# Kernel optimization log

Hardware: AMD Instinct MI355X
Metric: run time of the kernel (lower is better)

Reference implementation:

```python
import jax, jax.numpy as jnp
import numpy as np

B, N, D, H = 8, 1024, 768, 12
HD = D // H  # 64


def setup_inputs() -> dict:
    key = jax.random.key(0)
    ks = jax.random.split(key, 10)
    input_graph = jax.random.normal(ks[0], (B, N, D), dtype=jnp.float32)
    u = jax.random.uniform(ks[1], (B, N, N), dtype=jnp.float32)
    keep = jax.random.uniform(ks[2], (B, N, N)) < 0.15
    adj = jnp.where(keep, u, 0.0)
    s = 1.0 / np.sqrt(D)
    Wq = jax.random.normal(ks[3], (D, D), dtype=jnp.float32) * s
    bq = jnp.zeros((D,), dtype=jnp.float32)
    Wk = jax.random.normal(ks[4], (D, D), dtype=jnp.float32) * s
    bk = jnp.zeros((D,), dtype=jnp.float32)
    Wv = jax.random.normal(ks[5], (D, D), dtype=jnp.float32) * s
    bv = jnp.zeros((D,), dtype=jnp.float32)
    beta = jnp.asarray(0.1, dtype=jnp.float32)
    return {"input_graph": input_graph, "adj": adj, "Wq": Wq, "bq": bq,
            "Wk": Wk, "bk": bk, "Wv": Wv, "bv": bv, "beta": beta}


def _split_heads(x):
    # [B,N,D] -> [B,H,N,HD]
    b, n, _ = x.shape
    return x.reshape(b, n, H, HD).transpose(0, 2, 1, 3)


def reference(input_graph, adj, Wq, bq, Wk, bk, Wv, bv, beta):
    q = _split_heads(input_graph @ Wq + bq)  # [B,H,N,HD]
    k = _split_heads(input_graph @ Wk + bk)
    v = _split_heads(input_graph @ Wv + bv)
    scores = jnp.einsum('bhqd,bhkd->bhqk', q, k) / jnp.sqrt(jnp.asarray(HD, input_graph.dtype))
    adj_e = adj[:, None, :, :]  # [B,1,N,N]
    scores = scores + beta * adj_e
    scores = jnp.where(adj_e > 0, scores, jnp.asarray(-9e15, scores.dtype))
    probs = jax.nn.softmax(scores, axis=-1)
    out = jnp.einsum('bhqk,bhkd->bhqd', probs, v)  # [B,H,N,HD]
    return out.transpose(0, 2, 1, 3).reshape(input_graph.shape[0], input_graph.shape[1], D)
```

## Files before the change

### kernel.cpp

```cpp
#include <hip/hip_runtime.h>

#define B_ 8
#define N_ 1024
#define D_ 768
#define H_ 12
#define HD_ 64

#define LOG2E 1.4426950408889634f

typedef __attribute__((ext_vector_type(8))) short bf16x8;
typedef __attribute__((ext_vector_type(4))) short short4_t;
typedef __attribute__((ext_vector_type(4))) float f32x4;
typedef __attribute__((ext_vector_type(2))) unsigned int u32x2;
typedef unsigned int u32;

__device__ __forceinline__ short f2bf(float f) {
  union { float f; unsigned u; } v; v.f = f;
  unsigned u = v.u;
  unsigned r = u + 0x7fffu + ((u >> 16) & 1u);
  return (short)(r >> 16);
}
__device__ __forceinline__ float bf2f(short s) {
  union { unsigned u; float f; } v;
  v.u = ((unsigned)(unsigned short)s) << 16;
  return v.f;
}
__device__ __forceinline__ float bpermf(int srclane, float x) {
  union { float f; int i; } v; v.f = x;
  union { int i; float f; } r;
  r.i = __builtin_amdgcn_ds_bpermute(srclane * 4, v.i);
  return r.f;
}
__device__ __forceinline__ float max3f(float a, float b, float c) {
  return fmaxf(fmaxf(a, b), c);
}
__device__ __forceinline__ u32 cvtpk(float a, float b) {
  u32 r;
  asm("v_cvt_pk_bf16_f32 %0, %1, %2" : "=v"(r) : "v"(a), "v"(b));
  return r;
}

__device__ __forceinline__ void gload_lds16(const void* g, void* l) {
  __builtin_amdgcn_global_load_lds((const __attribute__((address_space(1))) u32*)g,
                                   (__attribute__((address_space(3))) u32*)l, 16, 0, 0);
}

__global__ __launch_bounds__(256)
void prep_kernel(const float* __restrict__ X, short* __restrict__ Xb,
                 const float* __restrict__ Wq, const float* __restrict__ Wk,
                 const float* __restrict__ Wv, short* __restrict__ Wt3,
                 const float* __restrict__ adj, const float* __restrict__ beta_p,
                 short* __restrict__ madjF) {
  const int bid = blockIdx.x;
  const int tid = threadIdx.x;

  if (bid < 3072) {
    int i = (bid * 256 + tid) * 8;
    float4 a = *(const float4*)(X + i);
    float4 b = *(const float4*)(X + i + 4);
    bf16x8 o;
    o[0] = f2bf(a.x); o[1] = f2bf(a.y); o[2] = f2bf(a.z); o[3] = f2bf(a.w);
    o[4] = f2bf(b.x); o[5] = f2bf(b.y); o[6] = f2bf(b.z); o[7] = f2bf(b.w);
    *(bf16x8*)(Xb + i) = o;
  } else if (bid < 4800) {
    const int i = bid - 3072;
    const int z = i / 576;
    const int rem = i % 576;
    const int bx = rem % 24, by = rem / 24;
    const float* W = z == 0 ? Wq : (z == 1 ? Wk : Wv);
    short* O = Wt3 + (size_t)z * D_ * D_;
    __shared__ float t[32][33];
    const int n0 = bx * 32, k0 = by * 32;
    const int tx = tid & 31, ty = tid >> 5;
#pragma unroll
    for (int j = 0; j < 4; j++)
      t[ty + 8 * j][tx] = W[(size_t)(k0 + ty + 8 * j) * D_ + n0 + tx];
    __syncthreads();
#pragma unroll
    for (int j = 0; j < 4; j++)
      O[(size_t)(n0 + ty + 8 * j) * D_ + k0 + tx] = f2bf(t[tx][ty + 8 * j]);
  } else {
    const int j = bid - 4800;
    const int b = j >> 8;
    const int rr = j & 255;
    const int qt = rr >> 4, kt = rr & 15;
    const float b2 = beta_p[0] * LOG2E;
    const float MASKV = -9.0e15f * LOG2E;

    __shared__ float Lt[64][68];
    {
      const int row = tid >> 2, cs = (tid & 3) * 16;
      const float* ap = adj + ((size_t)b * N_ + qt * 64 + row) * (size_t)N_ + kt * 64 + cs;
#pragma unroll
      for (int jj = 0; jj < 4; jj++)
        *(float4*)&Lt[row][cs + 4 * jj] = *(const float4*)(ap + 4 * jj);
    }
    __syncthreads();

    const int lane = tid & 63, w = tid >> 6;
    const int l15 = lane & 15, lg = lane >> 4;
    const int q = 16 * w + l15;
    short vals[16];
#pragma unroll
    for (int cb = 0; cb < 4; cb++) {
      float4 a4 = *(const float4*)&Lt[q][16 * cb + 4 * lg];
      float av[4] = {a4.x, a4.y, a4.z, a4.w};
#pragma unroll
      for (int r = 0; r < 4; r++) {
        float a = av[r];
        vals[cb * 4 + r] = f2bf((a > 0.f) ? b2 * a : MASKV);
      }
    }
    short* o = madjF + (((size_t)(b * 16 + qt) * 16 + kt) * 256 + tid) * 16;
    bf16x8 lo, hi;
#pragma unroll
    for (int jj = 0; jj < 8; jj++) { lo[jj] = vals[jj]; hi[jj] = vals[8 + jj]; }
    *(bf16x8*)o = lo;
    *(bf16x8*)(o + 8) = hi;
  }
}

__global__ __launch_bounds__(256, 4)
void qkv_gemm_kernel(const short* __restrict__ Xb, const short* __restrict__ Wt3,
                     const float* __restrict__ bq, const float* __restrict__ bk,
                     const float* __restrict__ bv, short* __restrict__ QKV) {
  const int z = blockIdx.z;
  const short* Wt = Wt3 + (size_t)z * D_ * D_;
  const float* bias = z == 0 ? bq : (z == 1 ? bk : bv);
  short* C = QKV + (size_t)z * (B_ * N_) * D_;
  const float alpha = (z == 0) ? 0.125f * LOG2E : 1.0f;

  const int m0 = blockIdx.x * 128;
  const int n0 = blockIdx.y * 128;
  const int tid = threadIdx.x;
  const int lane = tid & 63;
  const int wid = tid >> 6;
  const int wr = (wid >> 1) * 64;
  const int wc = (wid & 1) * 64;
  const int l15 = lane & 15;
  const int lg = lane >> 4;

  __shared__ short At[2][128][32];
  __shared__ short Bt[2][128][32];

  f32x4 acc[4][4];
#pragma unroll
  for (int m = 0; m < 4; m++)
#pragma unroll
    for (int n = 0; n < 4; n++)
      acc[m][n] = (f32x4){0.f, 0.f, 0.f, 0.f};

  const int srow_l = lane >> 2;
  const int sc8 = (((lane & 3) ^ ((lane >> 2) & 3)) * 8);
  const short* ag = Xb + (size_t)(m0 + wid * 16 + srow_l) * D_ + sc8;
  const short* bg = Wt + (size_t)(n0 + wid * 16 + srow_l) * D_ + sc8;

  auto stage = [&](int bi, int k0) {
#pragma unroll
    for (int p = 0; p < 2; p++) {
      gload_lds16(ag + (size_t)(64 * p) * D_ + k0,
                  ((short*)At[bi]) + (size_t)(wid + 4 * p) * 512);
      gload_lds16(bg + (size_t)(64 * p) * D_ + k0,
                  ((short*)Bt[bi]) + (size_t)(wid + 4 * p) * 512);
    }
  };

  stage(0, 0);
  for (int k0 = 0; k0 < D_; k0 += 32) {
    const int cur = (k0 >> 5) & 1;
    __syncthreads();
    if (k0 + 32 < D_) stage(cur ^ 1, k0 + 32);

    bf16x8 af[4], bfr[4];
#pragma unroll
    for (int m = 0; m < 4; m++) {
      const int row = wr + m * 16 + l15;
      af[m] = *(const bf16x8*)&At[cur][row][(lg ^ (l15 & 3)) * 8];
    }
#pragma unroll
    for (int n = 0; n < 4; n++) {
      const int row = wc + n * 16 + l15;
      bfr[n] = *(const bf16x8*)&Bt[cur][row][(lg ^ (l15 & 3)) * 8];
    }
#pragma unroll
    for (int m = 0; m < 4; m++)
#pragma unroll
      for (int n = 0; n < 4; n++)
        acc[m][n] = __builtin_amdgcn_mfma_f32_16x16x32_bf16(af[m], bfr[n], acc[m][n], 0, 0, 0);
  }

  if (z == 2) {
#pragma unroll
    for (int n = 0; n < 4; n++) {
      const int col = n0 + wc + n * 16 + l15;
      const float bval = bias[col];
      const int hh = col >> 6, dd = col & 63;
#pragma unroll
      for (int m = 0; m < 4; m++) {
        const int row = m0 + wr + m * 16 + 4 * lg;
        const int bb = row >> 10, nn = row & 1023;
        short4_t o;
#pragma unroll
        for (int r = 0; r < 4; r++) o[r] = f2bf(acc[m][n][r] + bval);
        *(short4_t*)&C[(((size_t)bb * H_ + hh) * HD_ + dd) * N_ + nn] = o;
      }
    }
  } else {
#pragma unroll
    for (int n = 0; n < 4; n++) {
      const int col = n0 + wc + n * 16 + l15;
      const float bval = bias[col];
#pragma unroll
      for (int m = 0; m < 4; m++) {
#pragma unroll
        for (int r = 0; r < 4; r++) {
          const int row = m0 + wr + m * 16 + 4 * lg + r;
          C[(size_t)row * D_ + col] = f2bf((acc[m][n][r] + bval) * alpha);
        }
      }
    }
  }
}

__global__ __launch_bounds__(512, 4)
void attn_kernel(const short* __restrict__ QKV, const short* __restrict__ madjF,
                 float* __restrict__ out) {
  const short* Qb = QKV;
  const short* Kb = QKV + (size_t)(B_ * N_) * D_;
  const short* VTg = QKV + 2 * (size_t)(B_ * N_) * D_;

  const int wg = blockIdx.x;
  const int b = wg & 7;
  const int rem = wg >> 3;
  const int h = rem >> 3;
  const int qt = rem & 7;

  const int tid = threadIdx.x;
  const int lane = tid & 63;
  const int w = tid >> 6;
  const int l15 = lane & 15;
  const int lg = lane >> 4;

  const int q0 = qt * 128;
  const size_t seq0 = (size_t)b * N_;
  const int hc = h * HD_;

  __shared__ short Kt[2][64][64];
  __shared__ short VTt[2][64][64];
  __shared__ short Pt[8][16][64];

  bf16x8 qf[2];
  {
    const short* qp = Qb + (seq0 + q0 + 16 * w + l15) * (size_t)D_ + hc + 8 * lg;
    qf[0] = *(const bf16x8*)qp;
    qf[1] = *(const bf16x8*)(qp + 32);
  }

  f32x4 acc[4];
#pragma unroll
  for (int cb = 0; cb < 4; cb++) acc[cb] = (f32x4){0.f, 0.f, 0.f, 0.f};
  float m_ = -__builtin_inff();
  float l_ = 0.f;

  const int srow = 8 * w + (lane >> 3);
  const int sc8 = ((lane & 7) ^ (lane >> 3)) * 8;
  const short* kg = Kb + (seq0 + srow) * (size_t)D_ + hc + sc8;
  const short* vg = VTg + ((size_t)(b * H_ + h) * HD_ + srow) * N_ + sc8;
  const int qm = 2 * qt + (w >> 2);
  const short* mg = madjF + ((size_t)(b * 16 + qm) * 16) * 4096 + ((w & 3) * 64 + lane) * 16;

  const int sw2 = (l15 & 7) << 1;
  char* ptrow = (char*)&Pt[w][l15][0];

  auto stage = [&](int bi, int kt) {
    const int k0 = kt * 64;
    gload_lds16(kg + (size_t)k0 * D_, ((short*)Kt[bi]) + (size_t)w * 512);
    gload_lds16(vg + k0, ((short*)VTt[bi]) + (size_t)w * 512);
  };

  stage(0, 0);
  bf16x8 mlo = *(const bf16x8*)mg;
  bf16x8 mhi = *(const bf16x8*)(mg + 8);

  for (int kt = 0; kt < 16; kt++) {
    const int cur = kt & 1;
    __syncthreads();
    if (kt < 15) stage(cur ^ 1, kt + 1);
    const int ktn = kt < 15 ? kt + 1 : 15;
    bf16x8 mlo2 = *(const bf16x8*)(mg + (size_t)ktn * 4096);
    bf16x8 mhi2 = *(const bf16x8*)(mg + (size_t)ktn * 4096 + 8);

    f32x4 s[4];
    __builtin_amdgcn_s_setprio(1);
#pragma unroll
    for (int cb = 0; cb < 4; cb++) {
      f32x4 c;
#pragma unroll
      for (int r = 0; r < 4; r++)
        c[r] = bf2f(cb < 2 ? mlo[(cb & 1) * 4 + r] : mhi[(cb & 1) * 4 + r]);
      const int swk = l15 & 7;
      bf16x8 kf0 = *(const bf16x8*)&Kt[cur][cb * 16 + l15][(lg ^ swk) * 8];
      bf16x8 kf1 = *(const bf16x8*)&Kt[cur][cb * 16 + l15][((lg + 4) ^ swk) * 8];
      c = __builtin_amdgcn_mfma_f32_16x16x32_bf16(kf0, qf[0], c, 0, 0, 0);
      s[cb] = __builtin_amdgcn_mfma_f32_16x16x32_bf16(kf1, qf[1], c, 0, 0, 0);
    }
    __builtin_amdgcn_s_setprio(0);
    mlo = mlo2; mhi = mhi2;

    float tm = max3f(max3f(s[0][0], s[0][1], s[0][2]),
                     max3f(s[0][3], s[1][0], s[1][1]),
                     max3f(s[1][2], s[1][3], s[2][0]));
    float tm2 = max3f(max3f(s[2][1], s[2][2], s[2][3]),
                      max3f(s[3][0], s[3][1], s[3][2]), s[3][3]);
    tm = fmaxf(tm, tm2);
    tm = fmaxf(tm, __shfl_xor(tm, 16));
    tm = fmaxf(tm, __shfl_xor(tm, 32));

    if (!__all(tm <= m_ + 8.f)) {
      const float mnew = fmaxf(m_, tm);
      const float sc2 = __builtin_exp2f(m_ - mnew);
      m_ = mnew;
      l_ *= sc2;
      float scr[4];
#pragma unroll
      for (int r = 0; r < 4; r++) scr[r] = bpermf(4 * lg + r, sc2);
#pragma unroll
      for (int cb = 0; cb < 4; cb++)
#pragma unroll
        for (int r = 0; r < 4; r++) acc[cb][r] *= scr[r];
    }

    float ps = 0.f;
    u32 pk[8];
#pragma unroll
    for (int cb = 0; cb < 4; cb++) {
#pragma unroll
      for (int rp = 0; rp < 2; rp++) {
        const float p0 = __builtin_exp2f(s[cb][2 * rp] - m_);
        const float p1 = __builtin_exp2f(s[cb][2 * rp + 1] - m_);
        ps += p0 + p1;
        pk[cb * 2 + rp] = cvtpk(p0, p1);
      }
    }
    ps += __shfl_xor(ps, 16);
    ps += __shfl_xor(ps, 32);
    l_ += ps;

#pragma unroll
    for (int cb = 0; cb < 4; cb++) {
      u32x2 wv = {pk[2 * cb], pk[2 * cb + 1]};
      *(u32x2*)(ptrow + (((4 * cb + lg) ^ sw2) << 3)) = wv;
    }

    __builtin_amdgcn_s_setprio(1);
#pragma unroll
    for (int ks = 0; ks < 2; ks++) {
      bf16x8 pa = *(const bf16x8*)(ptrow + ((((lg << 1) + 8 * ks) ^ sw2) << 3));
#pragma unroll
      for (int cb = 0; cb < 4; cb++) {
        const int row = cb * 16 + l15;
        bf16x8 vb = *(const bf16x8*)&VTt[cur][row][((lg + 4 * ks) ^ (row & 7)) * 8];
        acc[cb] = __builtin_amdgcn_mfma_f32_16x16x32_bf16(pa, vb, acc[cb], 0, 0, 0);
      }
    }
    __builtin_amdgcn_s_setprio(0);
  }

  float inv[4];
#pragma unroll
  for (int r = 0; r < 4; r++) inv[r] = 1.f / bpermf(4 * lg + r, l_);
#pragma unroll
  for (int cb = 0; cb < 4; cb++) {
#pragma unroll
    for (int r = 0; r < 4; r++) {
      out[(seq0 + q0 + 16 * w + 4 * lg + r) * (size_t)D_ + hc + cb * 16 + l15] =
          acc[cb][r] * inv[r];
    }
  }
}

extern "C" void kernel_launch(void* const* d_in, const int* in_sizes, int n_in,
                              void* d_out, int out_size, void* d_ws, size_t ws_size,
                              hipStream_t stream) {
  const float* X    = (const float*)d_in[0];
  const float* adj  = (const float*)d_in[1];
  const float* Wq   = (const float*)d_in[2];
  const float* bq   = (const float*)d_in[3];
  const float* Wk   = (const float*)d_in[4];
  const float* bk   = (const float*)d_in[5];
  const float* Wv   = (const float*)d_in[6];
  const float* bv   = (const float*)d_in[7];
  const float* beta = (const float*)d_in[8];
  float* out = (float*)d_out;

  short* Xb    = (short*)d_ws;
  short* Wt3   = Xb + (size_t)(B_ * N_) * D_;
  short* QKV   = Wt3 + 3 * (size_t)D_ * D_;
  short* madjF = QKV + 3 * (size_t)(B_ * N_) * D_;

  prep_kernel<<<dim3(6848), 256, 0, stream>>>(X, Xb, Wq, Wk, Wv, Wt3, adj, beta, madjF);
  qkv_gemm_kernel<<<dim3(64, 6, 3), 256, 0, stream>>>(Xb, Wt3, bq, bk, bv, QKV);
  attn_kernel<<<dim3(768), 512, 0, stream>>>(QKV, madjF, out);
}
```

Before: 126.5 us.

## Switch attention to 32x32x16 MFMA with register-resident P via permlane32 swap

Reworks the attention kernel to use 4 waves of 32 query rows each, computing S^T with 32x32x16 bf16 MFMAs so each lane owns one query row. The softmax probabilities are repacked in registers with v_permlane32_swap instead of going through an LDS P buffer, and row max/sum and rescaling no longer need bpermute. The adjacency-bias prep is reordered to match the new accumulator layout. Output stores become float4 vector writes. The trade-off is higher register pressure (fewer waves per block, occupancy hint of 3) and a correctness risk in the layout permutation.

```diff
diff --git a/kernel.cpp b/kernel.cpp
--- a/kernel.cpp
+++ b/kernel.cpp
@@ -11,7 +11,7 @@
 typedef __attribute__((ext_vector_type(8))) short bf16x8;
 typedef __attribute__((ext_vector_type(4))) short short4_t;
 typedef __attribute__((ext_vector_type(4))) float f32x4;
-typedef __attribute__((ext_vector_type(2))) unsigned int u32x2;
+typedef __attribute__((ext_vector_type(16))) float f32x16;
 typedef unsigned int u32;
 
 __device__ __forceinline__ short f2bf(float f) {
@@ -25,19 +25,13 @@
   v.u = ((unsigned)(unsigned short)s) << 16;
   return v.f;
 }
-__device__ __forceinline__ float bpermf(int srclane, float x) {
-  union { float f; int i; } v; v.f = x;
-  union { int i; float f; } r;
-  r.i = __builtin_amdgcn_ds_bpermute(srclane * 4, v.i);
-  return r.f;
-}
-__device__ __forceinline__ float max3f(float a, float b, float c) {
-  return fmaxf(fmaxf(a, b), c);
-}
 __device__ __forceinline__ u32 cvtpk(float a, float b) {
   u32 r;
   asm("v_cvt_pk_bf16_f32 %0, %1, %2" : "=v"(r) : "v"(a), "v"(b));
   return r;
+}
+__device__ __forceinline__ void pl32swap(u32& a, u32& b) {
+  asm("v_permlane32_swap_b32 %0, %1" : "+v"(a), "+v"(b));
 }
 
 __device__ __forceinline__ void gload_lds16(const void* g, void* l) {
@@ -83,35 +77,38 @@
     const int j = bid - 4800;
     const int b = j >> 8;
     const int rr = j & 255;
-    const int qt = rr >> 4, kt = rr & 15;
+    const int qt64 = rr >> 4, kt = rr & 15;
     const float b2 = beta_p[0] * LOG2E;
     const float MASKV = -9.0e15f * LOG2E;
 
     __shared__ float Lt[64][68];
     {
       const int row = tid >> 2, cs = (tid & 3) * 16;
-      const float* ap = adj + ((size_t)b * N_ + qt * 64 + row) * (size_t)N_ + kt * 64 + cs;
+      const float* ap = adj + ((size_t)b * N_ + qt64 * 64 + row) * (size_t)N_ + kt * 64 + cs;
 #pragma unroll
       for (int jj = 0; jj < 4; jj++)
         *(float4*)&Lt[row][cs + 4 * jj] = *(const float4*)(ap + 4 * jj);
     }
     __syncthreads();
 
-    const int lane = tid & 63, w = tid >> 6;
-    const int l15 = lane & 15, lg = lane >> 4;
-    const int q = 16 * w + l15;
+    const int a = tid >> 1, cb = tid & 1;
+    const int lane_att = a & 63;
+    const int l31 = lane_att & 31, hia = lane_att >> 5;
+    const int q_local = 32 * (a >> 6) + l31;
+
     short vals[16];
 #pragma unroll
-    for (int cb = 0; cb < 4; cb++) {
-      float4 a4 = *(const float4*)&Lt[q][16 * cb + 4 * lg];
+    for (int t = 0; t < 4; t++) {
+      float4 a4 = *(const float4*)&Lt[q_local][32 * cb + 8 * t + 4 * hia];
       float av[4] = {a4.x, a4.y, a4.z, a4.w};
 #pragma unroll
-      for (int r = 0; r < 4; r++) {
-        float a = av[r];
-        vals[cb * 4 + r] = f2bf((a > 0.f) ? b2 * a : MASKV);
+      for (int r2 = 0; r2 < 4; r2++) {
+        float av_ = av[r2];
+        vals[4 * t + r2] = f2bf((av_ > 0.f) ? b2 * av_ : MASKV);
       }
     }
-    short* o = madjF + (((size_t)(b * 16 + qt) * 16 + kt) * 256 + tid) * 16;
+    short* o = madjF + ((size_t)((b * 8 + (qt64 >> 1)) * 16 + kt)) * 8192 +
+               (qt64 & 1) * 4096 + tid * 16;
     bf16x8 lo, hi;
 #pragma unroll
     for (int jj = 0; jj < 8; jj++) { lo[jj] = vals[jj]; hi[jj] = vals[8 + jj]; }
@@ -222,7 +219,7 @@
   }
 }
 
-__global__ __launch_bounds__(512, 4)
+__global__ __launch_bounds__(256, 3)
 void attn_kernel(const short* __restrict__ QKV, const short* __restrict__ madjF,
                  float* __restrict__ out) {
   const short* Qb = QKV;
@@ -238,8 +235,9 @@
   const int tid = threadIdx.x;
   const int lane = tid & 63;
   const int w = tid >> 6;
-  const int l15 = lane & 15;
-  const int lg = lane >> 4;
+  const int l31 = lane & 31;
+  const int hi = lane >> 5;
+  const int swz = lane & 7;
 
   const int q0 = qt * 128;
   const size_t seq0 = (size_t)b * N_;
@@ -247,73 +245,77 @@
 
   __shared__ short Kt[2][64][64];
   __shared__ short VTt[2][64][64];
-  __shared__ short Pt[8][16][64];
-
-  bf16x8 qf[2];
+
+  bf16x8 qf[4];
   {
-    const short* qp = Qb + (seq0 + q0 + 16 * w + l15) * (size_t)D_ + hc + 8 * lg;
-    qf[0] = *(const bf16x8*)qp;
-    qf[1] = *(const bf16x8*)(qp + 32);
-  }
-
-  f32x4 acc[4];
-#pragma unroll
-  for (int cb = 0; cb < 4; cb++) acc[cb] = (f32x4){0.f, 0.f, 0.f, 0.f};
+    const short* qp = Qb + (seq0 + q0 + 32 * w + l31) * (size_t)D_ + hc + 8 * hi;
+#pragma unroll
+    for (int s = 0; s < 4; s++) qf[s] = *(const bf16x8*)(qp + 16 * s);
+  }
+
+  f32x16 acc0 = {}, acc1 = {};
   float m_ = -__builtin_inff();
   float l_ = 0.f;
 
-  const int srow = 8 * w + (lane >> 3);
+  const int srow = 16 * w + (lane >> 3);
   const int sc8 = ((lane & 7) ^ (lane >> 3)) * 8;
   const short* kg = Kb + (seq0 + srow) * (size_t)D_ + hc + sc8;
   const short* vg = VTg + ((size_t)(b * H_ + h) * HD_ + srow) * N_ + sc8;
-  const int qm = 2 * qt + (w >> 2);
-  const short* mg = madjF + ((size_t)(b * 16 + qm) * 16) * 4096 + ((w & 3) * 64 + lane) * 16;
-
-  const int sw2 = (l15 & 7) << 1;
-  char* ptrow = (char*)&Pt[w][l15][0];
+  const short* mg = madjF + ((size_t)(b * 8 + qt) * 16) * 8192 + (w * 64 + lane) * 32;
 
   auto stage = [&](int bi, int kt) {
     const int k0 = kt * 64;
-    gload_lds16(kg + (size_t)k0 * D_, ((short*)Kt[bi]) + (size_t)w * 512);
-    gload_lds16(vg + k0, ((short*)VTt[bi]) + (size_t)w * 512);
+    gload_lds16(kg + (size_t)k0 * D_, ((short*)Kt[bi]) + (size_t)w * 1024);
+    gload_lds16(kg + (size_t)(k0 + 8) * D_, ((short*)Kt[bi]) + (size_t)w * 1024 + 512);
+    gload_lds16(vg + k0, ((short*)VTt[bi]) + (size_t)w * 1024);
+    gload_lds16(vg + k0 + 8 * (size_t)N_, ((short*)VTt[bi]) + (size_t)w * 1024 + 512);
   };
 
   stage(0, 0);
-  bf16x8 mlo = *(const bf16x8*)mg;
-  bf16x8 mhi = *(const bf16x8*)(mg + 8);
+  bf16x8 mj[4];
+#pragma unroll
+  for (int j = 0; j < 4; j++) mj[j] = *(const bf16x8*)(mg + 8 * j);
 
   for (int kt = 0; kt < 16; kt++) {
     const int cur = kt & 1;
     __syncthreads();
     if (kt < 15) stage(cur ^ 1, kt + 1);
     const int ktn = kt < 15 ? kt + 1 : 15;
-    bf16x8 mlo2 = *(const bf16x8*)(mg + (size_t)ktn * 4096);
-    bf16x8 mhi2 = *(const bf16x8*)(mg + (size_t)ktn * 4096 + 8);
-
-    f32x4 s[4];
-    __builtin_amdgcn_s_setprio(1);
-#pragma unroll
-    for (int cb = 0; cb < 4; cb++) {
-      f32x4 c;
-#pragma unroll
-      for (int r = 0; r < 4; r++)
-        c[r] = bf2f(cb < 2 ? mlo[(cb & 1) * 4 + r] : mhi[(cb & 1) * 4 + r]);
-      const int swk = l15 & 7;
-      bf16x8 kf0 = *(const bf16x8*)&Kt[cur][cb * 16 + l15][(lg ^ swk) * 8];
-      bf16x8 kf1 = *(const bf16x8*)&Kt[cur][cb * 16 + l15][((lg + 4) ^ swk) * 8];
-      c = __builtin_amdgcn_mfma_f32_16x16x32_bf16(kf0, qf[0], c, 0, 0, 0);
-      s[cb] = __builtin_amdgcn_mfma_f32_16x16x32_bf16(kf1, qf[1], c, 0, 0, 0);
-    }
-    __builtin_amdgcn_s_setprio(0);
-    mlo = mlo2; mhi = mhi2;
-
-    float tm = max3f(max3f(s[0][0], s[0][1], s[0][2]),
-                     max3f(s[0][3], s[1][0], s[1][1]),
-                     max3f(s[1][2], s[1][3], s[2][0]));
-    float tm2 = max3f(max3f(s[2][1], s[2][2], s[2][3]),
-                      max3f(s[3][0], s[3][1], s[3][2]), s[3][3]);
-    tm = fmaxf(tm, tm2);
-    tm = fmaxf(tm, __shfl_xor(tm, 16));
+    bf16x8 mjn[4];
+#pragma unroll
+    for (int j = 0; j < 4; j++) mjn[j] = *(const bf16x8*)(mg + (size_t)ktn * 8192 + 8 * j);
+
+    f32x16 sA0, sA1;
+    {
+      f32x16 c;
+#pragma unroll
+      for (int r = 0; r < 16; r++) c[r] = bf2f(mj[r >> 3][r & 7]);
+#pragma unroll
+      for (int s = 0; s < 4; s++) {
+        bf16x8 kf = *(const bf16x8*)&Kt[cur][l31][((2 * s + hi) ^ swz) * 8];
+        c = __builtin_amdgcn_mfma_f32_32x32x16_bf16(kf, qf[s], c, 0, 0, 0);
+      }
+      sA0 = c;
+    }
+    {
+      f32x16 c;
+#pragma unroll
+      for (int r = 0; r < 16; r++) c[r] = bf2f(mj[2 + (r >> 3)][r & 7]);
+#pragma unroll
+      for (int s = 0; s < 4; s++) {
+        bf16x8 kf = *(const bf16x8*)&Kt[cur][32 + l31][((2 * s + hi) ^ swz) * 8];
+        c = __builtin_amdgcn_mfma_f32_32x32x16_bf16(kf, qf[s], c, 0, 0, 0);
+      }
+      sA1 = c;
+    }
+#pragma unroll
+    for (int j = 0; j < 4; j++) mj[j] = mjn[j];
+
+    float tm = sA0[0];
+#pragma unroll
+    for (int r = 1; r < 16; r++) tm = fmaxf(tm, sA0[r]);
+#pragma unroll
+    for (int r = 0; r < 16; r++) tm = fmaxf(tm, sA1[r]);
     tm = fmaxf(tm, __shfl_xor(tm, 32));
 
     if (!__all(tm <= m_ + 8.f)) {
@@ -321,61 +323,57 @@
       const float sc2 = __builtin_exp2f(m_ - mnew);
       m_ = mnew;
       l_ *= sc2;
-      float scr[4];
-#pragma unroll
-      for (int r = 0; r < 4; r++) scr[r] = bpermf(4 * lg + r, sc2);
-#pragma unroll
-      for (int cb = 0; cb < 4; cb++)
-#pragma unroll
-        for (int r = 0; r < 4; r++) acc[cb][r] *= scr[r];
+      acc0 = acc0 * sc2;
+      acc1 = acc1 * sc2;
     }
 
     float ps = 0.f;
-    u32 pk[8];
-#pragma unroll
-    for (int cb = 0; cb < 4; cb++) {
-#pragma unroll
-      for (int rp = 0; rp < 2; rp++) {
-        const float p0 = __builtin_exp2f(s[cb][2 * rp] - m_);
-        const float p1 = __builtin_exp2f(s[cb][2 * rp + 1] - m_);
-        ps += p0 + p1;
-        pk[cb * 2 + rp] = cvtpk(p0, p1);
-      }
-    }
-    ps += __shfl_xor(ps, 16);
+    u32 fw[16];
+    {
+#pragma unroll
+      for (int r = 0; r < 16; r++) { sA0[r] = __builtin_exp2f(sA0[r] - m_); ps += sA0[r]; }
+#pragma unroll
+      for (int r = 0; r < 16; r++) { sA1[r] = __builtin_exp2f(sA1[r] - m_); ps += sA1[r]; }
+      u32 w0[8], w1[8];
+#pragma unroll
+      for (int c = 0; c < 8; c++) w0[c] = cvtpk(sA0[2 * c], sA0[2 * c + 1]);
+#pragma unroll
+      for (int c = 0; c < 8; c++) w1[c] = cvtpk(sA1[2 * c], sA1[2 * c + 1]);
+      pl32swap(w0[0], w0[2]); fw[0] = w0[0];  fw[2] = w0[2];
+      pl32swap(w0[1], w0[3]); fw[1] = w0[1];  fw[3] = w0[3];
+      pl32swap(w0[4], w0[6]); fw[4] = w0[4];  fw[6] = w0[6];
+      pl32swap(w0[5], w0[7]); fw[5] = w0[5];  fw[7] = w0[7];
+      pl32swap(w1[0], w1[2]); fw[8] = w1[0];  fw[10] = w1[2];
+      pl32swap(w1[1], w1[3]); fw[9] = w1[1];  fw[11] = w1[3];
+      pl32swap(w1[4], w1[6]); fw[12] = w1[4]; fw[14] = w1[6];
+      pl32swap(w1[5], w1[7]); fw[13] = w1[5]; fw[15] = w1[7];
+    }
     ps += __shfl_xor(ps, 32);
     l_ += ps;
 
 #pragma unroll
-    for (int cb = 0; cb < 4; cb++) {
-      u32x2 wv = {pk[2 * cb], pk[2 * cb + 1]};
-      *(u32x2*)(ptrow + (((4 * cb + lg) ^ sw2) << 3)) = wv;
-    }
-
-    __builtin_amdgcn_s_setprio(1);
-#pragma unroll
-    for (int ks = 0; ks < 2; ks++) {
-      bf16x8 pa = *(const bf16x8*)(ptrow + ((((lg << 1) + 8 * ks) ^ sw2) << 3));
-#pragma unroll
-      for (int cb = 0; cb < 4; cb++) {
-        const int row = cb * 16 + l15;
-        bf16x8 vb = *(const bf16x8*)&VTt[cur][row][((lg + 4 * ks) ^ (row & 7)) * 8];
-        acc[cb] = __builtin_amdgcn_mfma_f32_16x16x32_bf16(pa, vb, acc[cb], 0, 0, 0);
-      }
-    }
-    __builtin_amdgcn_s_setprio(0);
-  }
-
-  float inv[4];
-#pragma unroll
-  for (int r = 0; r < 4; r++) inv[r] = 1.f / bpermf(4 * lg + r, l_);
-#pragma unroll
-  for (int cb = 0; cb < 4; cb++) {
-#pragma unroll
-    for (int r = 0; r < 4; r++) {
-      out[(seq0 + q0 + 16 * w + 4 * lg + r) * (size_t)D_ + hc + cb * 16 + l15] =
-          acc[cb][r] * inv[r];
-    }
+    for (int ks = 0; ks < 4; ks++) {
+      union { u32 u[4]; bf16x8 v; } pu;
+      pu.u[0] = fw[4 * ks]; pu.u[1] = fw[4 * ks + 1];
+      pu.u[2] = fw[4 * ks + 2]; pu.u[3] = fw[4 * ks + 3];
+      bf16x8 vf0 = *(const bf16x8*)&VTt[cur][l31][((2 * ks + hi) ^ swz) * 8];
+      bf16x8 vf1 = *(const bf16x8*)&VTt[cur][32 + l31][((2 * ks + hi) ^ swz) * 8];
+      acc0 = __builtin_amdgcn_mfma_f32_32x32x16_bf16(vf0, pu.v, acc0, 0, 0, 0);
+      acc1 = __builtin_amdgcn_mfma_f32_32x32x16_bf16(vf1, pu.v, acc1, 0, 0, 0);
+    }
+  }
+
+  const float invl = 1.f / l_;
+  float* orow = out + (seq0 + q0 + 32 * w + l31) * (size_t)D_ + hc;
+#pragma unroll
+  for (int t = 0; t < 4; t++) {
+    float4 o0, o1;
+    o0.x = acc0[4 * t] * invl;     o0.y = acc0[4 * t + 1] * invl;
+    o0.z = acc0[4 * t + 2] * invl; o0.w = acc0[4 * t + 3] * invl;
+    o1.x = acc1[4 * t] * invl;     o1.y = acc1[4 * t + 1] * invl;
+    o1.z = acc1[4 * t + 2] * invl; o1.w = acc1[4 * t + 3] * invl;
+    *(float4*)(orow + 8 * t + 4 * hi) = o0;
+    *(float4*)(orow + 8 * t + 4 * hi + 32) = o1;
   }
 }
 
@@ -400,5 +398,5 @@
 
   prep_kernel<<<dim3(6848), 256, 0, stream>>>(X, Xb, Wq, Wk, Wv, Wt3, adj, beta, madjF);
   qkv_gemm_kernel<<<dim3(64, 6, 3), 256, 0, stream>>>(Xb, Wt3, bq, bk, bv, QKV);
-  attn_kernel<<<dim3(768), 512, 0, stream>>>(QKV, madjF, out);
-}
+  attn_kernel<<<dim3(768), 256, 0, stream>>>(QKV, madjF, out);
+}
```

Result: faster. 120.3 us (-4.9%).
